# Optimization experiments

Hardware: AMD Instinct MI355X
Metric: run time of the kernel (lower is better)

The kernel has to match this reference:

```python
import jax, jax.numpy as jnp
import numpy as np

REPLACE = 4
REMAIN = 32
EPS = 1e-12


def _l2norm(x, axis):
    return x / jnp.maximum(jnp.linalg.norm(x, axis=axis, keepdims=True), EPS)


def setup_inputs() -> dict:
    key = jax.random.key(0)
    ks = jax.random.split(key, 16)
    B, d = 4096, 64
    n_users, n_entities, n_items = 100000, 200000, 50000
    K, n_cans, n_rel = 64, 64, 100
    return {
        "users": jax.random.randint(ks[0], (B,), 0, n_users),
        "items": jax.random.randint(ks[1], (B,), 0, n_items),
        "kg_neighbors": jax.random.randint(ks[2], (n_items, K), 0, n_entities),
        "all_candidates": jax.random.randint(ks[3], (n_rel, n_cans), 0, n_entities),
        "neighbor_relations": jax.random.randint(ks[4], (n_items, K), 0, n_rel),
        "user_all_embeddings": jax.random.normal(ks[5], (n_users, d), jnp.float32),
        "entity_all_embeddings": jax.random.normal(ks[6], (n_entities, d), jnp.float32),
        "item_embeddings": jax.random.normal(ks[7], (B, d), jnp.float32),
        "ui_W": jax.random.normal(ks[8], (2 * d, d), jnp.float32) / np.sqrt(2 * d),
        "ui_b": jnp.zeros((d,), jnp.float32),
        "e1_W": jax.random.normal(ks[9], (d, d), jnp.float32) / np.sqrt(d),
        "e1_b": jnp.zeros((d,), jnp.float32),
        "e2_W": jax.random.normal(ks[10], (d, d), jnp.float32) / np.sqrt(d),
        "e2_b": jnp.zeros((d,), jnp.float32),
    }


def reference(users, items, kg_neighbors, all_candidates, neighbor_relations,
              user_all_embeddings, entity_all_embeddings, item_embeddings,
              ui_W, ui_b, e1_W, e1_b, e2_W, e2_b):
    B = users.shape[0]
    d = user_all_embeddings.shape[1]
    idx_dtype = kg_neighbors.dtype

    neighbors = kg_neighbors[items]                      # [B, K]
    users_e = user_all_embeddings[users]                 # [B, d]
    ui_e = _l2norm(jnp.concatenate([users_e, item_embeddings], axis=1) @ ui_W + ui_b, 1)  # [B, d]

    # Step 1: score neighbors, pick top replace_num
    ne = _l2norm(entity_all_embeddings[neighbors] @ e1_W + e1_b, 2)   # [B, K, d]
    scores1 = jnp.einsum('bd,bkd->bk', ui_e, ne)
    logits1 = jax.nn.softmax(scores1, axis=1)
    step1_prob, step1_idx = jax.lax.top_k(logits1, REPLACE)          # [B, R]
    replaced = jnp.take_along_axis(neighbors, step1_idx, axis=1)     # [B, R]
    sel_rel = jnp.take_along_axis(neighbor_relations[items], step1_idx, axis=1)
    cf_kg1 = kg_neighbors.at[items[:, None], step1_idx].set(
        jnp.zeros((B, REPLACE), idx_dtype))
    ap1 = jnp.log(jnp.mean(step1_prob, axis=1))                      # [B]

    # Step 2: candidate pruning + sampling
    cands = all_candidates[sel_rel]                                  # [B, R, C]
    cands_e = entity_all_embeddings[cands]                           # [B, R, C, d]
    scores2 = jnp.einsum('bd,brcd->brc', users_e, cands_e)
    _, remain_idx = jax.lax.top_k(scores2, REMAIN)                   # [B, R, M]
    cands = jnp.take_along_axis(cands, remain_idx, axis=2).reshape(B * REPLACE, REMAIN)

    replaced_e = _l2norm(entity_all_embeddings[replaced] @ e1_W + e1_b, 2)
    replaced_e = replaced_e.reshape(B * REPLACE, d)
    cands_e2 = _l2norm(entity_all_embeddings[cands] @ e2_W + e2_b, 2)  # [BR, M, d]
    ui_rep = jnp.repeat(ui_e, REPLACE, axis=0)                         # [BR, d]
    s2 = jnp.einsum('nd,nmd->nm', ui_rep * replaced_e, cands_e2)       # [BR, M]
    logp2 = jax.nn.log_softmax(s2, axis=1)

    skey = jax.random.key(42)
    step2_idx = jax.random.categorical(skey, logp2, axis=1)           # [BR]
    rows = jnp.arange(B * REPLACE)
    step2_prob = jnp.exp(logp2[rows, step2_idx]).reshape(B, REPLACE)
    sel_ent = cands[rows, step2_idx].reshape(B, REPLACE)
    cf_kg2 = kg_neighbors.at[items[:, None], step1_idx].set(sel_ent.astype(idx_dtype))
    ap2 = jnp.log(jnp.mean(step1_prob, axis=1)) + jnp.log(jnp.mean(step2_prob, axis=1))
    return (cf_kg1, ap1, cf_kg2, ap2)
```

## Files before the change

### kernel.cpp

```cpp
#include <hip/hip_runtime.h>
#include <stdint.h>

#define EPS_NORM 1e-12f
#define F32_TINY 1.17549435e-38f

static __device__ __forceinline__ int rfl(int v) {
  return __builtin_amdgcn_readfirstlane(v);
}

__device__ __forceinline__ void threefry2x32(uint32_t k0, uint32_t k1,
                                             uint32_t x0, uint32_t x1,
                                             uint32_t& o0, uint32_t& o1) {
  uint32_t ks2 = k0 ^ k1 ^ 0x1BD11BDAu;
  x0 += k0; x1 += k1;
#define TF_ROT(r) { x0 += x1; x1 = (x1 << (r)) | (x1 >> (32 - (r))); x1 ^= x0; }
  TF_ROT(13) TF_ROT(15) TF_ROT(26) TF_ROT(6)
  x0 += k1; x1 += ks2 + 1u;
  TF_ROT(17) TF_ROT(29) TF_ROT(16) TF_ROT(24)
  x0 += ks2; x1 += k0 + 2u;
  TF_ROT(13) TF_ROT(15) TF_ROT(26) TF_ROT(6)
  x0 += k0; x1 += k1 + 3u;
  TF_ROT(17) TF_ROT(29) TF_ROT(16) TF_ROT(24)
  x0 += k1; x1 += ks2 + 4u;
  TF_ROT(13) TF_ROT(15) TF_ROT(26) TF_ROT(6)
  x0 += ks2; x1 += k0 + 5u;
#undef TF_ROT
  o0 = x0; o1 = x1;
}

__global__ __launch_bounds__(256, 3) void k_phase1(
    const float* __restrict__ E, const int* __restrict__ allc,
    const float* __restrict__ W1, const float* __restrict__ b1,
    const float* __restrict__ W2, const float* __restrict__ b2,
    const int* __restrict__ kg,
    float* __restrict__ T1, float* __restrict__ T2c, float* __restrict__ Eg,
    float* __restrict__ out0, int* __restrict__ wkg2) {
  __shared__ float Wl[4096];
  __shared__ float eT[4][2048];
  const int blk = blockIdx.x, tid = threadIdx.x;
  const int wv = tid >> 6, lane = tid & 63;
  const int NT1B = 1563, NT2B = 50;
  if (blk < NT1B + NT2B) {
    const bool isT1 = blk < NT1B;
    {
      const float* W = isT1 ? W1 : W2;
      for (int idx = tid; idx < 4096; idx += 256) {
        int k = idx >> 6, c = idx & 63;
        Wl[k * 64 + ((c & 7) * 8 + (c >> 3))] = W[idx];
      }
    }
    int rbase = (isT1 ? blk * 4 + wv : (blk - NT1B) * 4 + wv) * 32;
    bool active = !isT1 || rbase < 200000;
    int half = lane >> 5, r = lane & 31;
    if (active) {
      int srow = isT1 ? (rbase + r) : allc[rbase + r];
      const float4* Er =
          reinterpret_cast<const float4*>(E + (size_t)srow * 64 + half * 32);
      float4 c0 = Er[0], c1 = Er[1], c2 = Er[2], c3 = Er[3];
      float4 c4 = Er[4], c5 = Er[5], c6 = Er[6], c7 = Er[7];
      float ev[32] = {c0.x, c0.y, c0.z, c0.w, c1.x, c1.y, c1.z, c1.w,
                      c2.x, c2.y, c2.z, c2.w, c3.x, c3.y, c3.z, c3.w,
                      c4.x, c4.y, c4.z, c4.w, c5.x, c5.y, c5.z, c5.w,
                      c6.x, c6.y, c6.z, c6.w, c7.x, c7.y, c7.z, c7.w};
      float* et = eT[wv];
#pragma unroll
      for (int kk = 0; kk < 32; ++kk)
        et[(half * 32 + kk) * 32 + r] = ev[kk];
      if (!isT1) {
        float4* G =
            reinterpret_cast<float4*>(Eg + (size_t)(rbase + r) * 64 + half * 32);
        G[0] = c0; G[1] = c1; G[2] = c2; G[3] = c3;
        G[4] = c4; G[5] = c5; G[6] = c6; G[7] = c7;
      }
    }
    __syncthreads();
    if (!active) return;
    const int rg = lane >> 3, cg = lane & 7;
    float y[4][8];
#pragma unroll
    for (int ri = 0; ri < 4; ++ri)
#pragma unroll
      for (int ci = 0; ci < 8; ++ci) y[ri][ci] = 0.f;
    const float4* eT4 = reinterpret_cast<const float4*>(eT[wv]);
    const float4* W4 = reinterpret_cast<const float4*>(Wl);
#pragma unroll 8
    for (int k = 0; k < 64; ++k) {
      float4 e4 = eT4[k * 8 + rg];
      float4 wa = W4[k * 16 + cg * 2];
      float4 wb = W4[k * 16 + cg * 2 + 1];
      float ev4[4] = {e4.x, e4.y, e4.z, e4.w};
      float wv8[8] = {wa.x, wa.y, wa.z, wa.w, wb.x, wb.y, wb.z, wb.w};
#pragma unroll
      for (int ri = 0; ri < 4; ++ri)
#pragma unroll
        for (int ci = 0; ci < 8; ++ci)
          y[ri][ci] = fmaf(ev4[ri], wv8[ci], y[ri][ci]);
    }
    const float* bias = isT1 ? b1 : b2;
    float bv[8];
#pragma unroll
    for (int ci = 0; ci < 8; ++ci) bv[ci] = bias[ci * 8 + cg];
#pragma unroll
    for (int ri = 0; ri < 4; ++ri)
#pragma unroll
      for (int ci = 0; ci < 8; ++ci)
        y[ri][ci] = __fadd_rn(y[ri][ci], bv[ci]);
    float* dstB = isT1 ? T1 : T2c;
#pragma unroll
    for (int ri = 0; ri < 4; ++ri) {
      float A0 = __fadd_rn(__fmul_rn(y[ri][0], y[ri][0]),
                           __fmul_rn(y[ri][4], y[ri][4]));
      float A1 = __fadd_rn(__fmul_rn(y[ri][1], y[ri][1]),
                           __fmul_rn(y[ri][5], y[ri][5]));
      float A2 = __fadd_rn(__fmul_rn(y[ri][2], y[ri][2]),
                           __fmul_rn(y[ri][6], y[ri][6]));
      float A3 = __fadd_rn(__fmul_rn(y[ri][3], y[ri][3]),
                           __fmul_rn(y[ri][7], y[ri][7]));
      float B0 = __fadd_rn(A0, A2), B1 = __fadd_rn(A1, A3);
      float C = __fadd_rn(B0, B1);
      C = __fadd_rn(C, __shfl_xor(C, 4));
      C = __fadd_rn(C, __shfl_xor(C, 2));
      C = __fadd_rn(C, __shfl_xor(C, 1));
      float denom = fmaxf(sqrtf(C), EPS_NORM);
      float* drow = dstB + (size_t)(rbase + rg * 4 + ri) * 64;
#pragma unroll
      for (int ci = 0; ci < 8; ++ci) drow[ci * 8 + cg] = y[ri][ci] / denom;
    }
  } else {
    const int4* kg4 = reinterpret_cast<const int4*>(kg);
    float4* o4 = reinterpret_cast<float4*>(out0);
    int4* w4 = reinterpret_cast<int4*>(wkg2);
    for (int i = (blk - 1613) * 256 + tid; i < 800000; i += 200 * 256) {
      int4 v = kg4[i];
      o4[i] = make_float4((float)v.x, (float)v.y, (float)v.z, (float)v.w);
      w4[i] = v;
    }
  }
}

__global__ __launch_bounds__(256) void k_init(const int* __restrict__ kg,
                                              float* __restrict__ out0,
                                              int* __restrict__ wkg2, int n) {
  int i = blockIdx.x * 256 + threadIdx.x;
  if (i < n) { int v = kg[i]; out0[i] = (float)v; wkg2[i] = v; }
}

__device__ __forceinline__ void transform_row(const float4* __restrict__ Er,
                                              const float* __restrict__ W,
                                              const float* __restrict__ bias,
                                              float (&yn)[64]) {
  float y[64];
#pragma unroll
  for (int j = 0; j < 64; ++j) y[j] = 0.f;
  float4 c0 = Er[0], c1 = Er[1], c2 = Er[2], c3 = Er[3];
#pragma unroll 1
  for (int cc = 0; cc < 4; ++cc) {
    float4 n0, n1, n2, n3;
    if (cc < 3) { n0 = Er[cc * 4 + 4]; n1 = Er[cc * 4 + 5];
                  n2 = Er[cc * 4 + 6]; n3 = Er[cc * 4 + 7]; }
    float ev[16] = {c0.x, c0.y, c0.z, c0.w, c1.x, c1.y, c1.z, c1.w,
                    c2.x, c2.y, c2.z, c2.w, c3.x, c3.y, c3.z, c3.w};
#pragma unroll
    for (int k2i = 0; k2i < 16; ++k2i) {
      const float4* Wr = reinterpret_cast<const float4*>(
          W + ((size_t)(cc * 16 + k2i)) * 64);
      float ek = ev[k2i];
#pragma unroll
      for (int j4 = 0; j4 < 16; ++j4) {
        float4 w = Wr[j4];
        y[j4 * 4 + 0] = fmaf(ek, w.x, y[j4 * 4 + 0]);
        y[j4 * 4 + 1] = fmaf(ek, w.y, y[j4 * 4 + 1]);
        y[j4 * 4 + 2] = fmaf(ek, w.z, y[j4 * 4 + 2]);
        y[j4 * 4 + 3] = fmaf(ek, w.w, y[j4 * 4 + 3]);
      }
    }
    c0 = n0; c1 = n1; c2 = n2; c3 = n3;
  }
  const float4* B4 = reinterpret_cast<const float4*>(bias);
#pragma unroll
  for (int j4 = 0; j4 < 16; ++j4) {
    float4 bb = B4[j4];
    float bv[4] = {bb.x, bb.y, bb.z, bb.w};
#pragma unroll
    for (int t = 0; t < 4; ++t) y[j4 * 4 + t] = __fadd_rn(y[j4 * 4 + t], bv[t]);
  }
  float S1[32];
#pragma unroll
  for (int i = 0; i < 32; ++i)
    S1[i] = __fadd_rn(__fmul_rn(y[i], y[i]), __fmul_rn(y[i + 32], y[i + 32]));
#pragma unroll
  for (int i = 0; i < 16; ++i) S1[i] = __fadd_rn(S1[i], S1[i + 16]);
#pragma unroll
  for (int i = 0; i < 8; ++i)  S1[i] = __fadd_rn(S1[i], S1[i + 8]);
#pragma unroll
  for (int i = 0; i < 4; ++i)  S1[i] = __fadd_rn(S1[i], S1[i + 4]);
#pragma unroll
  for (int i = 0; i < 2; ++i)  S1[i] = __fadd_rn(S1[i], S1[i + 2]);
  float ss = __fadd_rn(S1[0], S1[1]);
  float denom = fmaxf(sqrtf(ss), EPS_NORM);
#pragma unroll
  for (int j = 0; j < 64; ++j) yn[j] = y[j] / denom;
}

__global__ __launch_bounds__(256) void k_transform64(
    const float* __restrict__ src, const int* __restrict__ gidx,
    const float* __restrict__ W, const float* __restrict__ bias,
    float* __restrict__ out, int nrows) {
  __shared__ float Wl[4096];
  for (int i = threadIdx.x; i < 4096; i += 256) Wl[i] = W[i];
  __syncthreads();
  int wid = threadIdx.x >> 6, lane = threadIdx.x & 63;
  int row = rfl(blockIdx.x * 4 + wid);
  if (row >= nrows) return;
  int srow = rfl(gidx ? gidx[row] : row);
  const float* er = src + (size_t)srow * 64;
  float y = 0.f;
#pragma unroll
  for (int k = 0; k < 64; ++k) y = fmaf(er[k], Wl[k * 64 + lane], y);
  y += bias[lane];
  float ss = y * y;
#pragma unroll
  for (int off = 32; off; off >>= 1) ss += __shfl_xor(ss, off);
  float yn = y / fmaxf(sqrtf(ss), EPS_NORM);
  out[(size_t)row * 64 + lane] = yn;
}

__global__ __launch_bounds__(256) void k_ui(
    const float* __restrict__ U, const int* __restrict__ users,
    const float* __restrict__ Iemb, const float* __restrict__ W,
    const float* __restrict__ bias, float* __restrict__ out, int B) {
  __shared__ float Wl[8192];
  for (int i = threadIdx.x; i < 8192; i += 256) Wl[i] = W[i];
  __syncthreads();
  int wid = threadIdx.x >> 6, lane = threadIdx.x & 63;
  int b = rfl(blockIdx.x * 4 + wid);
  if (b >= B) return;
  int usr = rfl(users[b]);
  const float* ur = U + (size_t)usr * 64;
  const float* ir = Iemb + (size_t)b * 64;
  float y = 0.f;
#pragma unroll
  for (int k = 0; k < 64; ++k) y = fmaf(ur[k], Wl[k * 64 + lane], y);
#pragma unroll
  for (int k = 0; k < 64; ++k) y = fmaf(ir[k], Wl[(64 + k) * 64 + lane], y);
  y += bias[lane];
  float ss = y * y;
#pragma unroll
  for (int off = 32; off; off >>= 1) ss += __shfl_xor(ss, off);
  float yn = y / fmaxf(sqrtf(ss), EPS_NORM);
  out[(size_t)b * 64 + lane] = yn;
}

__device__ __forceinline__ void score1_tail(
    float s, int lane, int b, int item, int nb,
    const int* __restrict__ nrel,
    float* __restrict__ out0, float* __restrict__ ap1_out,
    int* __restrict__ s1_idx, int* __restrict__ s1_rel, int* __restrict__ s1_ent,
    float* __restrict__ lmp1) {
  float m = s;
#pragma unroll
  for (int off = 32; off; off >>= 1) m = fmaxf(m, __shfl_xor(m, off));
  float ex = expf(s - m);
  float sum = ex;
#pragma unroll
  for (int off = 32; off; off >>= 1) sum += __shfl_xor(sum, off);
  float p = ex / sum;
  int rank = 0;
  for (int k2 = 0; k2 < 64; ++k2) {
    float pv = __shfl(p, k2);
    rank += (pv > p || (pv == p && k2 < lane)) ? 1 : 0;
  }
  float acc = 0.f;
#pragma unroll
  for (int rr = 0; rr < 4; ++rr) {
    unsigned long long msk = __ballot(rank == rr);
    int src = __ffsll(msk) - 1;
    acc += __shfl(p, src);
  }
  float lm = logf(acc * 0.25f);
  if (lane == 0) { ap1_out[b] = lm; lmp1[b] = lm; }
  if (rank < 4) {
    s1_idx[b * 4 + rank] = lane;
    s1_ent[b * 4 + rank] = nb;
    s1_rel[b * 4 + rank] = nrel[(size_t)item * 64 + lane];
    out0[(size_t)item * 64 + lane] = 0.0f;
  }
}

__global__ __launch_bounds__(256) void k_score1g(
    const int* __restrict__ items, const int* __restrict__ kg,
    const int* __restrict__ nrel, const float* __restrict__ T1,
    const float* __restrict__ uiE,
    float* __restrict__ out0, float* __restrict__ ap1_out,
    int* __restrict__ s1_idx, int* __restrict__ s1_rel, int* __restrict__ s1_ent,
    float* __restrict__ lmp1) {
  int tid = threadIdx.x, wv = tid >> 6, lane = tid & 63;
  int b = rfl(blockIdx.x * 4 + wv);
  int item = rfl(items[b]);
  int nb = kg[(size_t)item * 64 + lane];
  const float4* R = reinterpret_cast<const float4*>(T1 + (size_t)nb * 64);
  float yn[64];
#pragma unroll
  for (int j4 = 0; j4 < 16; ++j4) {
    float4 v = R[j4];
    yn[4 * j4] = v.x; yn[4 * j4 + 1] = v.y; yn[4 * j4 + 2] = v.z; yn[4 * j4 + 3] = v.w;
  }
  const float4* Ur = reinterpret_cast<const float4*>(uiE + (size_t)b * 64);
  float D[32];
#pragma unroll
  for (int i4 = 0; i4 < 8; ++i4) {
    float4 ua = Ur[i4], ub = Ur[i4 + 8];
    float uav[4] = {ua.x, ua.y, ua.z, ua.w};
    float ubv[4] = {ub.x, ub.y, ub.z, ub.w};
#pragma unroll
    for (int t = 0; t < 4; ++t) {
      int i = i4 * 4 + t;
      D[i] = __fadd_rn(__fmul_rn(yn[i], uav[t]), __fmul_rn(yn[i + 32], ubv[t]));
    }
  }
#pragma unroll
  for (int i = 0; i < 16; ++i) D[i] = __fadd_rn(D[i], D[i + 16]);
#pragma unroll
  for (int i = 0; i < 8; ++i)  D[i] = __fadd_rn(D[i], D[i + 8]);
#pragma unroll
  for (int i = 0; i < 4; ++i)  D[i] = __fadd_rn(D[i], D[i + 4]);
#pragma unroll
  for (int i = 0; i < 2; ++i)  D[i] = __fadd_rn(D[i], D[i + 2]);
  float s = __fadd_rn(D[0], D[1]);
  score1_tail(s, lane, b, item, nb, nrel, out0, ap1_out, s1_idx, s1_rel, s1_ent, lmp1);
}

__global__ __launch_bounds__(256) void k_score1(
    const int* __restrict__ items, const int* __restrict__ kg,
    const int* __restrict__ nrel, const float* __restrict__ E,
    const float* __restrict__ W1, const float* __restrict__ b1,
    const float* __restrict__ uiE,
    float* __restrict__ out0, float* __restrict__ ap1_out,
    int* __restrict__ s1_idx, int* __restrict__ s1_rel, int* __restrict__ s1_ent,
    float* __restrict__ lmp1) {
  int tid = threadIdx.x, wv = tid >> 6, lane = tid & 63;
  int b = rfl(blockIdx.x * 4 + wv);
  int item = rfl(items[b]);
  int nb = kg[(size_t)item * 64 + lane];
  const float4* Er = reinterpret_cast<const float4*>(E + (size_t)nb * 64);
  float yn[64];
  transform_row(Er, W1, b1, yn);
  const float4* Ur = reinterpret_cast<const float4*>(uiE + (size_t)b * 64);
  float D[32];
#pragma unroll
  for (int i4 = 0; i4 < 8; ++i4) {
    float4 ua = Ur[i4], ub = Ur[i4 + 8];
    float uav[4] = {ua.x, ua.y, ua.z, ua.w};
    float ubv[4] = {ub.x, ub.y, ub.z, ub.w};
#pragma unroll
    for (int t = 0; t < 4; ++t) {
      int i = i4 * 4 + t;
      D[i] = __fadd_rn(__fmul_rn(yn[i], uav[t]), __fmul_rn(yn[i + 32], ubv[t]));
    }
  }
#pragma unroll
  for (int i = 0; i < 16; ++i) D[i] = __fadd_rn(D[i], D[i + 16]);
#pragma unroll
  for (int i = 0; i < 8; ++i)  D[i] = __fadd_rn(D[i], D[i + 8]);
#pragma unroll
  for (int i = 0; i < 4; ++i)  D[i] = __fadd_rn(D[i], D[i + 4]);
#pragma unroll
  for (int i = 0; i < 2; ++i)  D[i] = __fadd_rn(D[i], D[i + 2]);
  float s = __fadd_rn(D[0], D[1]);
  score1_tail(s, lane, b, item, nb, nrel, out0, ap1_out, s1_idx, s1_rel, s1_ent, lmp1);
}

__global__ __launch_bounds__(256) void k_score2e(
    const int* __restrict__ users, const int* __restrict__ s1_rel,
    const float* __restrict__ U, const float* __restrict__ Eg,
    const int* __restrict__ allc, int* __restrict__ kept, int N) {
  int wid = threadIdx.x >> 6, lane = threadIdx.x & 63;
  int n = rfl(blockIdx.x * 4 + wid);
  if (n >= N) return;
  int b = n >> 2;
  int rel = rfl(s1_rel[n]);
  int usr = rfl(users[b]);
  int ent = allc[rel * 64 + lane];
  const float* ur = U + (size_t)usr * 64;
  const float4* e4 = reinterpret_cast<const float4*>(Eg + ((size_t)rel * 64 + lane) * 64);
  float s = 0.f;
#pragma unroll
  for (int j4 = 0; j4 < 16; ++j4) {
    float4 t = e4[j4];
    s = fmaf(ur[4 * j4 + 0], t.x, s);
    s = fmaf(ur[4 * j4 + 1], t.y, s);
    s = fmaf(ur[4 * j4 + 2], t.z, s);
    s = fmaf(ur[4 * j4 + 3], t.w, s);
  }
  int rank = 0;
  for (int k2 = 0; k2 < 64; ++k2) {
    float sv = __shfl(s, k2);
    rank += (sv > s || (sv == s && k2 < lane)) ? 1 : 0;
  }
  if (rank < 32) kept[n * 32 + rank] = (lane << 18) | ent;
}

__global__ __launch_bounds__(256) void k_score2(
    const int* __restrict__ users, const int* __restrict__ s1_rel,
    const float* __restrict__ U, const float* __restrict__ E,
    const int* __restrict__ allc, int* __restrict__ kept, int N) {
  int wid = threadIdx.x >> 6, lane = threadIdx.x & 63;
  int n = rfl(blockIdx.x * 4 + wid);
  if (n >= N) return;
  int b = n >> 2;
  int rel = rfl(s1_rel[n]);
  int usr = rfl(users[b]);
  int ent = allc[rel * 64 + lane];
  const float* ur = U + (size_t)usr * 64;
  const float4* e4 = reinterpret_cast<const float4*>(E + (size_t)ent * 64);
  float s = 0.f;
#pragma unroll
  for (int j4 = 0; j4 < 16; ++j4) {
    float4 t = e4[j4];
    s = fmaf(ur[4 * j4 + 0], t.x, s);
    s = fmaf(ur[4 * j4 + 1], t.y, s);
    s = fmaf(ur[4 * j4 + 2], t.z, s);
    s = fmaf(ur[4 * j4 + 3], t.w, s);
  }
  int rank = 0;
  for (int k2 = 0; k2 < 64; ++k2) {
    float sv = __shfl(s, k2);
    rank += (sv > s || (sv == s && k2 < lane)) ? 1 : 0;
  }
  if (rank < 32) kept[n * 32 + rank] = (lane << 18) | ent;
}

__device__ __forceinline__ void sample_body(
    float q, int n, int b, int lane,
    const int* __restrict__ items, const int* __restrict__ s1_idx,
    int rel, const float* __restrict__ T2c, const int* __restrict__ kept,
    float* __restrict__ p2, int* __restrict__ wkg2) {
  int m = lane & 31;
  int pk = kept[n * 32 + m];
  int c = pk >> 18;
  int ent = pk & 0x3FFFF;
  const float4* c4 = reinterpret_cast<const float4*>(T2c + ((size_t)rel * 64 + c) * 64);
  float s = 0.f;
#pragma unroll
  for (int j4 = 0; j4 < 16; ++j4) {
    float4 t = c4[j4];
    s = fmaf(__shfl(q, 4 * j4 + 0), t.x, s);
    s = fmaf(__shfl(q, 4 * j4 + 1), t.y, s);
    s = fmaf(__shfl(q, 4 * j4 + 2), t.z, s);
    s = fmaf(__shfl(q, 4 * j4 + 3), t.w, s);
  }
  float mx = s;
#pragma unroll
  for (int off = 1; off < 32; off <<= 1) mx = fmaxf(mx, __shfl_xor(mx, off));
  float shv = s - mx;
  float se = expf(shv);
  float sum = se;
#pragma unroll
  for (int off = 1; off < 32; off <<= 1) sum += __shfl_xor(sum, off);
  float logp = shv - logf(sum);
  uint32_t h0, h1;
  threefry2x32(0u, 42u, 0u, (uint32_t)(n * 32 + m), h0, h1);
  uint32_t bits = h0 ^ h1;
  float u0 = __uint_as_float((bits >> 9) | 0x3F800000u) - 1.0f;
  float uu = fmaxf(u0, F32_TINY);
  float g = -logf(-logf(uu));
  float z = g + logp;
  float bz = z; int bm = m;
#pragma unroll
  for (int off = 1; off < 32; off <<= 1) {
    float oz = __shfl_xor(bz, off);
    int om = __shfl_xor(bm, off);
    if (oz > bz || (oz == bz && om < bm)) { bz = oz; bm = om; }
  }
  if (lane == bm) {
    p2[n] = expf(logp);
    int col = s1_idx[n];
    int item = items[b];
    atomicMax(&wkg2[(size_t)item * 64 + col], ((b + 1) << 18) | ent);
  }
}

__global__ __launch_bounds__(256) void k_sample2(
    const int* __restrict__ items,
    const int* __restrict__ s1_idx, const int* __restrict__ s1_rel,
    const int* __restrict__ s1_ent, const float* __restrict__ T1,
    const float* __restrict__ T2c, const float* __restrict__ uiE,
    const int* __restrict__ kept,
    float* __restrict__ p2, int* __restrict__ wkg2, int N) {
  int tid = threadIdx.x, wid = tid >> 6, lane = tid & 63;
  int n = rfl(blockIdx.x * 4 + wid);
  if (n >= N) return;
  int b = n >> 2;
  int rel = rfl(s1_rel[n]);
  int repl = rfl(s1_ent[n]);
  float q = uiE[(size_t)b * 64 + lane] * T1[(size_t)repl * 64 + lane];
  sample_body(q, n, b, lane, items, s1_idx, rel, T2c, kept, p2, wkg2);
}

__global__ __launch_bounds__(256) void k_sample(
    const int* __restrict__ items,
    const int* __restrict__ s1_idx, const int* __restrict__ s1_rel,
    const int* __restrict__ s1_ent,
    const float* __restrict__ E, const float* __restrict__ W1,
    const float* __restrict__ b1, const float* __restrict__ T2c,
    const float* __restrict__ uiE, const int* __restrict__ kept,
    float* __restrict__ p2, int* __restrict__ wkg2, int N) {
  __shared__ float Wl[4096];
  int tid = threadIdx.x;
  for (int i = tid; i < 4096; i += 256) Wl[i] = W1[i];
  __syncthreads();
  int wid = tid >> 6, lane = tid & 63;
  int n = rfl(blockIdx.x * 4 + wid);
  if (n >= N) return;
  int b = n >> 2;
  int rel = rfl(s1_rel[n]);
  int repl = rfl(s1_ent[n]);
  const float* er = E + (size_t)repl * 64;
  float y = 0.f;
#pragma unroll
  for (int k2 = 0; k2 < 64; ++k2) y = fmaf(er[k2], Wl[k2 * 64 + lane], y);
  y += b1[lane];
  float ss = y * y;
#pragma unroll
  for (int off = 32; off; off >>= 1) ss += __shfl_xor(ss, off);
  float yn = y / fmaxf(sqrtf(ss), EPS_NORM);
  float q = uiE[(size_t)b * 64 + lane] * yn;
  sample_body(q, n, b, lane, items, s1_idx, rel, T2c, kept, p2, wkg2);
}

__global__ __launch_bounds__(256) void k_fin(const int* __restrict__ wkg2,
                                             const float* __restrict__ p2,
                                             const float* __restrict__ lmp1,
                                             float* __restrict__ out2,
                                             float* __restrict__ out3,
                                             int n, int B) {
  int i = blockIdx.x * 256 + threadIdx.x;
  if (i < n) out2[i] = (float)(wkg2[i] & 0x3FFFF);
  if (i < B) {
    float a = ((p2[i * 4] + p2[i * 4 + 1]) + p2[i * 4 + 2]) + p2[i * 4 + 3];
    out3[i] = lmp1[i] + logf(a * 0.25f);
  }
}

extern "C" void kernel_launch(void* const* d_in, const int* in_sizes, int n_in,
                              void* d_out, int out_size, void* d_ws, size_t ws_size,
                              hipStream_t stream) {
  const int*   users = (const int*)d_in[0];
  const int*   items = (const int*)d_in[1];
  const int*   kg    = (const int*)d_in[2];
  const int*   allc  = (const int*)d_in[3];
  const int*   nrel  = (const int*)d_in[4];
  const float* U     = (const float*)d_in[5];
  const float* E     = (const float*)d_in[6];
  const float* Iemb  = (const float*)d_in[7];
  const float* uiW   = (const float*)d_in[8];
  const float* uib   = (const float*)d_in[9];
  const float* e1W   = (const float*)d_in[10];
  const float* e1b   = (const float*)d_in[11];
  const float* e2W   = (const float*)d_in[12];
  const float* e2b   = (const float*)d_in[13];

  const int B = 4096, NCELL = 3200000, NCAND = 6400, NR4 = 16384, NENT = 200000;

  float* out0    = (float*)d_out;
  float* out_ap1 = out0 + NCELL;
  float* out2    = out_ap1 + B;
  float* out_ap2 = out2 + NCELL;

  float* T2c  = (float*)d_ws;
  float* uiE  = T2c + 409600;
  int*   wkg2 = (int*)(uiE + 262144);
  int*   s1i  = wkg2 + NCELL;
  int*   s1r  = s1i + NR4;
  int*   s1e  = s1r + NR4;
  int*   kept = s1e + NR4;
  float* p2   = (float*)(kept + 524288);
  float* lmp1 = p2 + NR4;
  float* T1   = lmp1 + B;
  float* Eg   = out2;
  const size_t WS_NEED = ((size_t)(T1 + (size_t)NENT * 64) - (size_t)d_ws);
  const bool pathA = ws_size >= WS_NEED;

  if (pathA) {
    k_phase1<<<1813, 256, 0, stream>>>(E, allc, e1W, e1b, e2W, e2b, kg,
                                       T1, T2c, Eg, out0, wkg2);
    k_ui<<<(B + 3) / 4, 256, 0, stream>>>(U, users, Iemb, uiW, uib, uiE, B);
    k_score1g<<<B / 4, 256, 0, stream>>>(items, kg, nrel, T1, uiE,
                                         out0, out_ap1, s1i, s1r, s1e, lmp1);
    k_score2e<<<(NR4 + 3) / 4, 256, 0, stream>>>(users, s1r, U, Eg, allc, kept, NR4);
    k_sample2<<<(NR4 + 3) / 4, 256, 0, stream>>>(items, s1i, s1r, s1e, T1, T2c,
                                                 uiE, kept, p2, wkg2, NR4);
  } else {
    k_init<<<(NCELL + 255) / 256, 256, 0, stream>>>(kg, out0, wkg2, NCELL);
    k_ui<<<(B + 3) / 4, 256, 0, stream>>>(U, users, Iemb, uiW, uib, uiE, B);
    k_transform64<<<(NCAND + 3) / 4, 256, 0, stream>>>(E, allc, e2W, e2b, T2c, NCAND);
    k_score1<<<B / 4, 256, 0, stream>>>(items, kg, nrel, E, e1W, e1b, uiE,
                                        out0, out_ap1, s1i, s1r, s1e, lmp1);
    k_score2<<<(NR4 + 3) / 4, 256, 0, stream>>>(users, s1r, U, E, allc, kept, NR4);
    k_sample<<<(NR4 + 3) / 4, 256, 0, stream>>>(items, s1i, s1r, s1e, E, e1W, e1b,
                                                T2c, uiE, kept, p2, wkg2, NR4);
  }
  k_fin<<<(NCELL + 255) / 256, 256, 0, stream>>>(wkg2, p2, lmp1, out2, out_ap2,
                                                 NCELL, B);
}
```

Baseline: 138.4 us.

## Fuse ui projection into phase1, halve blocks, permute T1 layout for vector stores

Folds the user-item projection kernel into the phase-1 kernel as an extra block range, removing one launch and letting it overlap with the entity transform. Each transform block now processes two 128-row batches with a smaller shared buffer, reusing the loaded weight tile, and raises occupancy by staging only half a row at a time. T1 is stored in a permuted column order so writes become float4, and downstream readers (score1g, sample2) undo the permutation through index remapping. This adds more loop iterations per block and relies on the permutation being applied consistently in every consumer.

```diff
diff --git a/kernel.cpp b/kernel.cpp
--- a/kernel.cpp
+++ b/kernel.cpp
@@ -28,109 +28,145 @@
   o0 = x0; o1 = x1;
 }
 
-__global__ __launch_bounds__(256, 3) void k_phase1(
+#define PERM_IDX(p) ((((p) & 7) << 3) | ((p) >> 3))
+
+__global__ __launch_bounds__(256, 5) void k_phase1(
     const float* __restrict__ E, const int* __restrict__ allc,
     const float* __restrict__ W1, const float* __restrict__ b1,
     const float* __restrict__ W2, const float* __restrict__ b2,
-    const int* __restrict__ kg,
+    const float* __restrict__ U, const int* __restrict__ users,
+    const float* __restrict__ Iemb, const float* __restrict__ uiW,
+    const float* __restrict__ uib, const int* __restrict__ kg,
     float* __restrict__ T1, float* __restrict__ T2c, float* __restrict__ Eg,
-    float* __restrict__ out0, int* __restrict__ wkg2) {
-  __shared__ float Wl[4096];
-  __shared__ float eT[4][2048];
+    float* __restrict__ uiE, float* __restrict__ out0, int* __restrict__ wkg2) {
+  __shared__ float SM[8192];
   const int blk = blockIdx.x, tid = threadIdx.x;
   const int wv = tid >> 6, lane = tid & 63;
-  const int NT1B = 1563, NT2B = 50;
+  const int NT1B = 782, NT2B = 25, NUIB = 256;
   if (blk < NT1B + NT2B) {
     const bool isT1 = blk < NT1B;
     {
       const float* W = isT1 ? W1 : W2;
       for (int idx = tid; idx < 4096; idx += 256) {
         int k = idx >> 6, c = idx & 63;
-        Wl[k * 64 + ((c & 7) * 8 + (c >> 3))] = W[idx];
-      }
-    }
-    int rbase = (isT1 ? blk * 4 + wv : (blk - NT1B) * 4 + wv) * 32;
-    bool active = !isT1 || rbase < 200000;
-    int half = lane >> 5, r = lane & 31;
-    if (active) {
-      int srow = isT1 ? (rbase + r) : allc[rbase + r];
-      const float4* Er =
-          reinterpret_cast<const float4*>(E + (size_t)srow * 64 + half * 32);
-      float4 c0 = Er[0], c1 = Er[1], c2 = Er[2], c3 = Er[3];
-      float4 c4 = Er[4], c5 = Er[5], c6 = Er[6], c7 = Er[7];
-      float ev[32] = {c0.x, c0.y, c0.z, c0.w, c1.x, c1.y, c1.z, c1.w,
-                      c2.x, c2.y, c2.z, c2.w, c3.x, c3.y, c3.z, c3.w,
-                      c4.x, c4.y, c4.z, c4.w, c5.x, c5.y, c5.z, c5.w,
-                      c6.x, c6.y, c6.z, c6.w, c7.x, c7.y, c7.z, c7.w};
-      float* et = eT[wv];
-#pragma unroll
-      for (int kk = 0; kk < 32; ++kk)
-        et[(half * 32 + kk) * 32 + r] = ev[kk];
-      if (!isT1) {
-        float4* G =
-            reinterpret_cast<float4*>(Eg + (size_t)(rbase + r) * 64 + half * 32);
-        G[0] = c0; G[1] = c1; G[2] = c2; G[3] = c3;
-        G[4] = c4; G[5] = c5; G[6] = c6; G[7] = c7;
+        SM[k * 64 + ((c & 7) * 8 + (c >> 3))] = W[idx];
       }
     }
     __syncthreads();
-    if (!active) return;
     const int rg = lane >> 3, cg = lane & 7;
-    float y[4][8];
-#pragma unroll
-    for (int ri = 0; ri < 4; ++ri)
-#pragma unroll
-      for (int ci = 0; ci < 8; ++ci) y[ri][ci] = 0.f;
-    const float4* eT4 = reinterpret_cast<const float4*>(eT[wv]);
-    const float4* W4 = reinterpret_cast<const float4*>(Wl);
-#pragma unroll 8
-    for (int k = 0; k < 64; ++k) {
-      float4 e4 = eT4[k * 8 + rg];
-      float4 wa = W4[k * 16 + cg * 2];
-      float4 wb = W4[k * 16 + cg * 2 + 1];
-      float ev4[4] = {e4.x, e4.y, e4.z, e4.w};
-      float wv8[8] = {wa.x, wa.y, wa.z, wa.w, wb.x, wb.y, wb.z, wb.w};
-#pragma unroll
-      for (int ri = 0; ri < 4; ++ri)
-#pragma unroll
-        for (int ci = 0; ci < 8; ++ci)
-          y[ri][ci] = fmaf(ev4[ri], wv8[ci], y[ri][ci]);
-    }
+    const int sub = lane >> 5, r = lane & 31;
     const float* bias = isT1 ? b1 : b2;
     float bv[8];
 #pragma unroll
     for (int ci = 0; ci < 8; ++ci) bv[ci] = bias[ci * 8 + cg];
-#pragma unroll
-    for (int ri = 0; ri < 4; ++ri)
-#pragma unroll
-      for (int ci = 0; ci < 8; ++ci)
-        y[ri][ci] = __fadd_rn(y[ri][ci], bv[ci]);
-    float* dstB = isT1 ? T1 : T2c;
-#pragma unroll
-    for (int ri = 0; ri < 4; ++ri) {
-      float A0 = __fadd_rn(__fmul_rn(y[ri][0], y[ri][0]),
-                           __fmul_rn(y[ri][4], y[ri][4]));
-      float A1 = __fadd_rn(__fmul_rn(y[ri][1], y[ri][1]),
-                           __fmul_rn(y[ri][5], y[ri][5]));
-      float A2 = __fadd_rn(__fmul_rn(y[ri][2], y[ri][2]),
-                           __fmul_rn(y[ri][6], y[ri][6]));
-      float A3 = __fadd_rn(__fmul_rn(y[ri][3], y[ri][3]),
-                           __fmul_rn(y[ri][7], y[ri][7]));
-      float B0 = __fadd_rn(A0, A2), B1 = __fadd_rn(A1, A3);
-      float C = __fadd_rn(B0, B1);
-      C = __fadd_rn(C, __shfl_xor(C, 4));
-      C = __fadd_rn(C, __shfl_xor(C, 2));
-      C = __fadd_rn(C, __shfl_xor(C, 1));
-      float denom = fmaxf(sqrtf(C), EPS_NORM);
-      float* drow = dstB + (size_t)(rbase + rg * 4 + ri) * 64;
-#pragma unroll
-      for (int ci = 0; ci < 8; ++ci) drow[ci * 8 + cg] = y[ri][ci] / denom;
+    float* eTw = SM + 4096 + wv * 1024;
+    const float4* eT4 = reinterpret_cast<const float4*>(eTw);
+    const float4* W4 = reinterpret_cast<const float4*>(SM);
+#pragma unroll 1
+    for (int t = 0; t < 2; ++t) {
+      int batch = (isT1 ? blk : blk - NT1B) * 2 + t;
+      int rbase = batch * 128 + wv * 32;
+      if (isT1 && rbase >= 200000) continue;
+      int srow = isT1 ? (rbase + r) : allc[rbase + r];
+      const float4* Er = reinterpret_cast<const float4*>(E + (size_t)srow * 64);
+      float y[4][8];
+#pragma unroll
+      for (int ri = 0; ri < 4; ++ri)
+#pragma unroll
+        for (int ci = 0; ci < 8; ++ci) y[ri][ci] = 0.f;
+#pragma unroll 1
+      for (int h = 0; h < 2; ++h) {
+        float4 a0 = Er[h * 8 + sub * 4 + 0];
+        float4 a1 = Er[h * 8 + sub * 4 + 1];
+        float4 a2 = Er[h * 8 + sub * 4 + 2];
+        float4 a3 = Er[h * 8 + sub * 4 + 3];
+        float ev[16] = {a0.x, a0.y, a0.z, a0.w, a1.x, a1.y, a1.z, a1.w,
+                        a2.x, a2.y, a2.z, a2.w, a3.x, a3.y, a3.z, a3.w};
+#pragma unroll
+        for (int kk = 0; kk < 16; ++kk)
+          eTw[(sub * 16 + kk) * 32 + r] = ev[kk];
+        if (!isT1) {
+          float4* G = reinterpret_cast<float4*>(
+              Eg + (size_t)(rbase + r) * 64 + h * 32 + sub * 16);
+          G[0] = a0; G[1] = a1; G[2] = a2; G[3] = a3;
+        }
+#pragma unroll 8
+        for (int kk = 0; kk < 32; ++kk) {
+          float4 e4 = eT4[kk * 8 + rg];
+          float4 wa = W4[(h * 32 + kk) * 16 + cg * 2];
+          float4 wb = W4[(h * 32 + kk) * 16 + cg * 2 + 1];
+          float ev4[4] = {e4.x, e4.y, e4.z, e4.w};
+          float wv8[8] = {wa.x, wa.y, wa.z, wa.w, wb.x, wb.y, wb.z, wb.w};
+#pragma unroll
+          for (int ri = 0; ri < 4; ++ri)
+#pragma unroll
+            for (int ci = 0; ci < 8; ++ci)
+              y[ri][ci] = fmaf(ev4[ri], wv8[ci], y[ri][ci]);
+        }
+      }
+#pragma unroll
+      for (int ri = 0; ri < 4; ++ri)
+#pragma unroll
+        for (int ci = 0; ci < 8; ++ci)
+          y[ri][ci] = __fadd_rn(y[ri][ci], bv[ci]);
+#pragma unroll
+      for (int ri = 0; ri < 4; ++ri) {
+        float A0 = __fadd_rn(__fmul_rn(y[ri][0], y[ri][0]),
+                             __fmul_rn(y[ri][4], y[ri][4]));
+        float A1 = __fadd_rn(__fmul_rn(y[ri][1], y[ri][1]),
+                             __fmul_rn(y[ri][5], y[ri][5]));
+        float A2 = __fadd_rn(__fmul_rn(y[ri][2], y[ri][2]),
+                             __fmul_rn(y[ri][6], y[ri][6]));
+        float A3 = __fadd_rn(__fmul_rn(y[ri][3], y[ri][3]),
+                             __fmul_rn(y[ri][7], y[ri][7]));
+        float B0 = __fadd_rn(A0, A2), B1 = __fadd_rn(A1, A3);
+        float C = __fadd_rn(B0, B1);
+        C = __fadd_rn(C, __shfl_xor(C, 4));
+        C = __fadd_rn(C, __shfl_xor(C, 2));
+        C = __fadd_rn(C, __shfl_xor(C, 1));
+        float denom = fmaxf(sqrtf(C), EPS_NORM);
+        int row = rbase + rg * 4 + ri;
+        if (isT1) {
+          float4* drow = reinterpret_cast<float4*>(T1 + (size_t)row * 64 + cg * 8);
+          drow[0] = make_float4(y[ri][0] / denom, y[ri][1] / denom,
+                                y[ri][2] / denom, y[ri][3] / denom);
+          drow[1] = make_float4(y[ri][4] / denom, y[ri][5] / denom,
+                                y[ri][6] / denom, y[ri][7] / denom);
+        } else {
+          float* drow = T2c + (size_t)row * 64;
+#pragma unroll
+          for (int ci = 0; ci < 8; ++ci) drow[ci * 8 + cg] = y[ri][ci] / denom;
+        }
+      }
+    }
+  } else if (blk < NT1B + NT2B + NUIB) {
+    int ub = blk - (NT1B + NT2B);
+    for (int i = tid; i < 8192; i += 256) SM[i] = uiW[i];
+    __syncthreads();
+    float bl = uib[lane];
+#pragma unroll 1
+    for (int t = 0; t < 4; ++t) {
+      int b = ub * 16 + wv * 4 + t;
+      int usr = rfl(users[b]);
+      const float* ur = U + (size_t)usr * 64;
+      const float* ir = Iemb + (size_t)b * 64;
+      float y = 0.f;
+#pragma unroll
+      for (int k = 0; k < 64; ++k) y = fmaf(ur[k], SM[k * 64 + lane], y);
+#pragma unroll
+      for (int k = 0; k < 64; ++k) y = fmaf(ir[k], SM[(64 + k) * 64 + lane], y);
+      y += bl;
+      float ss = y * y;
+#pragma unroll
+      for (int off = 32; off; off >>= 1) ss += __shfl_xor(ss, off);
+      float yn = y / fmaxf(sqrtf(ss), EPS_NORM);
+      uiE[(size_t)b * 64 + lane] = yn;
     }
   } else {
     const int4* kg4 = reinterpret_cast<const int4*>(kg);
     float4* o4 = reinterpret_cast<float4*>(out0);
     int4* w4 = reinterpret_cast<int4*>(wkg2);
-    for (int i = (blk - 1613) * 256 + tid; i < 800000; i += 200 * 256) {
+    for (int i = (blk - 1063) * 256 + tid; i < 800000; i += 200 * 256) {
       int4 v = kg4[i];
       o4[i] = make_float4((float)v.x, (float)v.y, (float)v.z, (float)v.w);
       w4[i] = v;
@@ -301,9 +337,12 @@
   const float4* R = reinterpret_cast<const float4*>(T1 + (size_t)nb * 64);
   float yn[64];
 #pragma unroll
-  for (int j4 = 0; j4 < 16; ++j4) {
-    float4 v = R[j4];
-    yn[4 * j4] = v.x; yn[4 * j4 + 1] = v.y; yn[4 * j4 + 2] = v.z; yn[4 * j4 + 3] = v.w;
+  for (int p4 = 0; p4 < 16; ++p4) {
+    float4 v = R[p4];
+    yn[PERM_IDX(4 * p4 + 0)] = v.x;
+    yn[PERM_IDX(4 * p4 + 1)] = v.y;
+    yn[PERM_IDX(4 * p4 + 2)] = v.z;
+    yn[PERM_IDX(4 * p4 + 3)] = v.w;
   }
   const float4* Ur = reinterpret_cast<const float4*>(uiE + (size_t)b * 64);
   float D[32];
@@ -430,6 +469,7 @@
   if (rank < 32) kept[n * 32 + rank] = (lane << 18) | ent;
 }
 
+template <bool PERMQ>
 __device__ __forceinline__ void sample_body(
     float q, int n, int b, int lane,
     const int* __restrict__ items, const int* __restrict__ s1_idx,
@@ -444,10 +484,10 @@
 #pragma unroll
   for (int j4 = 0; j4 < 16; ++j4) {
     float4 t = c4[j4];
-    s = fmaf(__shfl(q, 4 * j4 + 0), t.x, s);
-    s = fmaf(__shfl(q, 4 * j4 + 1), t.y, s);
-    s = fmaf(__shfl(q, 4 * j4 + 2), t.z, s);
-    s = fmaf(__shfl(q, 4 * j4 + 3), t.w, s);
+    s = fmaf(__shfl(q, PERMQ ? PERM_IDX(4 * j4 + 0) : (4 * j4 + 0)), t.x, s);
+    s = fmaf(__shfl(q, PERMQ ? PERM_IDX(4 * j4 + 1) : (4 * j4 + 1)), t.y, s);
+    s = fmaf(__shfl(q, PERMQ ? PERM_IDX(4 * j4 + 2) : (4 * j4 + 2)), t.z, s);
+    s = fmaf(__shfl(q, PERMQ ? PERM_IDX(4 * j4 + 3) : (4 * j4 + 3)), t.w, s);
   }
   float mx = s;
 #pragma unroll
@@ -493,8 +533,9 @@
   int b = n >> 2;
   int rel = rfl(s1_rel[n]);
   int repl = rfl(s1_ent[n]);
-  float q = uiE[(size_t)b * 64 + lane] * T1[(size_t)repl * 64 + lane];
-  sample_body(q, n, b, lane, items, s1_idx, rel, T2c, kept, p2, wkg2);
+  int pl = PERM_IDX(lane);
+  float q = uiE[(size_t)b * 64 + pl] * T1[(size_t)repl * 64 + lane];
+  sample_body<true>(q, n, b, lane, items, s1_idx, rel, T2c, kept, p2, wkg2);
 }
 
 __global__ __launch_bounds__(256) void k_sample(
@@ -525,7 +566,7 @@
   for (int off = 32; off; off >>= 1) ss += __shfl_xor(ss, off);
   float yn = y / fmaxf(sqrtf(ss), EPS_NORM);
   float q = uiE[(size_t)b * 64 + lane] * yn;
-  sample_body(q, n, b, lane, items, s1_idx, rel, T2c, kept, p2, wkg2);
+  sample_body<false>(q, n, b, lane, items, s1_idx, rel, T2c, kept, p2, wkg2);
 }
 
 __global__ __launch_bounds__(256) void k_fin(const int* __restrict__ wkg2,
@@ -582,9 +623,9 @@
   const bool pathA = ws_size >= WS_NEED;
 
   if (pathA) {
-    k_phase1<<<1813, 256, 0, stream>>>(E, allc, e1W, e1b, e2W, e2b, kg,
-                                       T1, T2c, Eg, out0, wkg2);
-    k_ui<<<(B + 3) / 4, 256, 0, stream>>>(U, users, Iemb, uiW, uib, uiE, B);
+    k_phase1<<<1263, 256, 0, stream>>>(E, allc, e1W, e1b, e2W, e2b, U, users,
+                                       Iemb, uiW, uib, kg, T1, T2c, Eg, uiE,
+                                       out0, wkg2);
     k_score1g<<<B / 4, 256, 0, stream>>>(items, kg, nrel, T1, uiE,
                                          out0, out_ap1, s1i, s1r, s1e, lmp1);
     k_score2e<<<(NR4 + 3) / 4, 256, 0, stream>>>(users, s1r, U, Eg, allc, kept, NR4);
```

New measurement: 163.9 us. 1.18x slower.
